# Optimization experiments

Hardware: AMD Instinct MI355X
Metric: run time of the kernel (lower is better)

The kernel has to match this reference:

```python
import jax, jax.numpy as jnp
import numpy as np

B, T, C_IN, H, W = 8, 12, 64, 64, 64
HID = 128
K = 3
NUM_CLASSES = 5


def _conv2d(x, w, b):
    # x: (B, Cin, H, W), w: (Cout, Cin, k, k) -> (B, Cout, H, W), SAME padding
    y = jax.lax.conv_general_dilated(
        x, w, window_strides=(1, 1), padding='SAME',
        dimension_numbers=('NCHW', 'OIHW', 'NCHW'))
    return y + b[None, :, None, None]


def setup_inputs() -> dict:
    key = jax.random.key(0)
    ks = jax.random.split(key, 5)
    inputs = jax.random.normal(ks[0], (B, T, C_IN, H, W), dtype=jnp.float32)
    # ConvLSTM gate conv: concat(x, h) channels -> 4*hidden gate channels
    fan_in = (C_IN + HID) * K * K
    w_lstm = jax.random.normal(ks[1], (4 * HID, C_IN + HID, K, K), dtype=jnp.float32) / np.sqrt(fan_in)
    b_lstm = jnp.zeros((4 * HID,), dtype=jnp.float32)
    w_conv = jax.random.normal(ks[2], (NUM_CLASSES, HID, K, K), dtype=jnp.float32) / np.sqrt(HID * K * K)
    b_conv = jnp.zeros((NUM_CLASSES,), dtype=jnp.float32)
    return {'inputs': inputs, 'w_lstm': w_lstm, 'b_lstm': b_lstm,
            'w_conv': w_conv, 'b_conv': b_conv}


def _clstm(inputs, w_lstm, b_lstm):
    # inputs: (B, T, C, H, W); returns final hidden state (B, HID, H, W)
    xs = jnp.transpose(inputs, (1, 0, 2, 3, 4))  # (T, B, C, H, W)
    h0 = jnp.zeros((inputs.shape[0], HID, H, W), dtype=inputs.dtype)
    c0 = jnp.zeros_like(h0)

    def step(carry, x_t):
        h, c = carry
        combined = jnp.concatenate([x_t, h], axis=1)           # (B, C+HID, H, W)
        gates = _conv2d(combined, w_lstm, b_lstm)              # (B, 4*HID, H, W)
        cc_i, cc_f, cc_o, cc_g = jnp.split(gates, 4, axis=1)
        i = jax.nn.sigmoid(cc_i)
        f = jax.nn.sigmoid(cc_f)
        o = jax.nn.sigmoid(cc_o)
        g = jnp.tanh(cc_g)
        c_next = f * c + i * g
        h_next = o * jnp.tanh(c_next)
        return (h_next, c_next), None

    (h_T, _), _ = jax.lax.scan(step, (h0, c0), xs)
    return h_T


def reference(inputs, w_lstm, b_lstm, w_conv, b_conv):
    final_state = _clstm(inputs, w_lstm, b_lstm)               # (B, HID, H, W)
    scores = _conv2d(final_state, w_conv, b_conv)              # (B, NUM_CLASSES, H, W)
    # Softmax2d over channels followed by log == channelwise log_softmax
    preds = jax.nn.log_softmax(scores, axis=1)
    return preds
```

## Files before the change

### kernel.cpp

```cpp
#include <hip/hip_runtime.h>
#include <math.h>

#define BB   8
#define TT   12

typedef _Float16 f16;
typedef f16  f16x8 __attribute__((ext_vector_type(8)));
typedef float f32x4 __attribute__((ext_vector_type(4)));

#define OFF_WT2  0ull
#define OFF_WC   1818624ull
#define OFF_XP   1855488ull
#define OFF_HA   6451200ull
#define OFF_HB   15642624ull
#define OFF_C    24834048ull
#define WS_END   41611264ull
#define ZERO_BYTES (WS_END - OFF_XP)

#define A_BYTES 43008
#define B_BYTES 37888

__device__ inline void gload16(const void* g, void* l) {
    __builtin_amdgcn_global_load_lds((const __attribute__((address_space(1))) void*)g,
                                     (__attribute__((address_space(3))) void*)l, 16, 0, 0);
}

__device__ inline float sigm_fast(float x) {
    return 1.f / (1.f + __expf(-x));
}
__device__ inline float tanh_fast(float x) {
    float xx = fminf(fmaxf(x, -15.f), 15.f);
    float e = __expf(2.f * xx);
    return (e - 1.f) / (e + 1.f);
}

__global__ __launch_bounds__(256) void zero_kernel(float4* __restrict__ p, int n4) {
    int i = blockIdx.x * blockDim.x + threadIdx.x;
    int stride = gridDim.x * blockDim.x;
    for (; i < n4; i += stride) p[i] = make_float4(0.f, 0.f, 0.f, 0.f);
}

__global__ __launch_bounds__(256) void wprep(const float* __restrict__ w, f16* __restrict__ wT2) {
    int t = blockIdx.x * 256 + threadIdx.x;
    if (t >= 8 * 6 * 64 * 296) return;
    int k    = t % 296;
    int r    = t / 296;
    int co_l = r & 63;
    int r2   = r >> 6;
    int chunk = r2 % 6;
    int ntl   = r2 / 6;
    f16 val = (f16)0.f;
    if (k < 288) {
        int tap = k >> 5, ci_l = k & 31;
        int ci  = chunk * 32 + ci_l;
        int cop = ntl * 64 + co_l;
        int hid = cop >> 2, gate = cop & 3;
        val = (f16)w[((size_t)(gate * 128 + hid) * 192 + ci) * 9 + tap];
    }
    wT2[t] = val;
}

__global__ __launch_bounds__(256) void wcprep(const float* __restrict__ w, float* __restrict__ wc) {
    int t = blockIdx.x * 256 + threadIdx.x;
    if (t >= 9216) return;
    int cls = t & 7, ci = (t >> 3) & 127, tap = t >> 10;
    wc[t] = (cls < 5) ? w[(size_t)(cls * 128 + ci) * 9 + tap] : 0.f;
}

__global__ __launch_bounds__(256) void xprep(const float* __restrict__ x, f16* __restrict__ xp, int t) {
    int pos = blockIdx.x * 256 + threadIdx.x;
    int b = pos >> 12, rr = pos & 4095, y = rr >> 6, xx = rr & 63;
    const float* s = x + ((size_t)(b * TT + t) * 64) * 4096 + y * 64 + xx;
    f16* d = xp + (((size_t)b * 66 + y + 1) * 68 + xx + 1) * 64;
    #pragma unroll
    for (int c8 = 0; c8 < 8; ++c8) {
        f16x8 v;
        #pragma unroll
        for (int e = 0; e < 8; ++e) v[e] = (f16)s[(size_t)(c8 * 8 + e) * 4096];
        *(f16x8*)&d[c8 * 8] = v;
    }
}

__device__ inline float pickc(f32x4 v, int j) {
    return j == 0 ? v[0] : j == 1 ? v[1] : j == 2 ? v[2] : v[3];
}

__global__ __launch_bounds__(256, 1) void gemm_step(
    const f16* __restrict__ xp, const f16* __restrict__ hin,
    const f16* __restrict__ wT2, const float* __restrict__ b_lstm,
    float* __restrict__ c_st, f16* __restrict__ hout)
{
    __shared__ __align__(16) char smem[2 * A_BYTES + 2 * B_BYTES];
    char* Ab0 = smem;
    char* Ab1 = smem + A_BYTES;
    char* Bb0 = smem + 2 * A_BYTES;
    char* Bb1 = smem + 2 * A_BYTES + B_BYTES;

    const int tid  = threadIdx.x;
    const int lane = tid & 63;
    const int wid  = tid >> 6;
    const int l15  = lane & 15, lg = lane >> 4;

    const int bid = blockIdx.x;
    const int nt  = bid >> 6;
    const int mt  = bid & 63;
    const int b   = mt >> 3;
    const int yr  = (mt & 7) << 3;

    const int rowbase = (b * 66 + yr) * 68;
    const f16* wslice = wT2 + (size_t)(nt * 6) * 18944;

    f32x4 acc[8][4] = {};

    int poA[11], cxA[11];
    #pragma unroll
    for (int i = 0; i < 11; ++i) {
        int k = wid + i * 4;
        int item = k * 64 + lane;
        int pc = item >> 2;
        int s  = item & 3;
        int pcc = pc < 660 ? pc : 0;
        int r = (pcc * 497) >> 15;
        int c = pcc - r * 66;
        poA[i] = rowbase + r * 68 + c;
        cxA[i] = (s ^ ((pcc >> 1) & 3)) * 8;
    }

    auto stageA = [&](int cc, char* Ad) {
        const f16* act; int sh, ci0;
        if (cc < 2) { act = xp;  sh = 6; ci0 = cc * 32; }
        else        { act = hin; sh = 7; ci0 = cc * 32 - 64; }
        #pragma unroll
        for (int i = 0; i < 11; ++i) {
            int k = wid + i * 4;
            if (k < 42)
                gload16(act + (((size_t)poA[i]) << sh) + ci0 + cxA[i], Ad + k * 1024);
        }
    };
    auto stageB = [&](int cc, char* Bd) {
        const char* bsrc = (const char*)(wslice + (size_t)cc * 18944);
        for (int k = wid; k < 37; k += 4)
            gload16(bsrc + k * 1024 + lane * 16, Bd + k * 1024);
    };
    auto compute = [&](const char* Abuf, const char* Bbuf) {
        const f16* As  = (const f16*)Abuf;
        const f16* Bsf = (const f16*)Bbuf;
        #pragma unroll
        for (int tap = 0; tap < 9; ++tap) {
            const int dy = tap / 3, dx = tap - dy * 3;
            f16x8 a[8];
            #pragma unroll
            for (int r2 = 0; r2 < 2; ++r2)
                #pragma unroll
                for (int mf = 0; mf < 4; ++mf) {
                    int p = (wid * 2 + r2 + dy) * 66 + mf * 16 + l15 + dx;
                    a[r2 * 4 + mf] = *(const f16x8*)&As[p * 32 + ((lg ^ ((p >> 1) & 3)) << 3)];
                }
            f16x8 bf[4];
            #pragma unroll
            for (int nf = 0; nf < 4; ++nf)
                bf[nf] = *(const f16x8*)&Bsf[(nf * 16 + l15) * 296 + tap * 32 + lg * 8];
            #pragma unroll
            for (int m = 0; m < 8; ++m)
                #pragma unroll
                for (int nf = 0; nf < 4; ++nf)
                    acc[m][nf] = __builtin_amdgcn_mfma_f32_16x16x32_f16(a[m], bf[nf], acc[m][nf], 0, 0, 0);
        }
    };

    stageA(0, Ab0);
    stageB(0, Bb0);
    __syncthreads();

    char* Ac = Ab0; char* Aa = Ab1;
    char* Bc = Bb0; char* Ba = Bb1;

    #pragma unroll 1
    for (int cc = 0; cc < 6; ++cc) {
        if (cc < 5) {
            stageA(cc + 1, Aa);
            stageB(cc + 1, Ba);
        }
        compute(Ac, Bc);
        __syncthreads();
        char* t1 = Ac; Ac = Aa; Aa = t1;
        char* t2 = Bc; Bc = Ba; Ba = t2;
    }

    const int q = lane & 3;
    #pragma unroll
    for (int m = 0; m < 8; ++m) {
        const int r2 = m >> 2, mf = m & 3;
        #pragma unroll
        for (int nf = 0; nf < 4; ++nf) {
            int hid = nt * 16 + nf * 4 + (l15 >> 2);
            float bias = b_lstm[q * 128 + hid];
            f32x4 v = acc[m][nf];
            v[0] += bias; v[1] += bias; v[2] += bias; v[3] += bias;
            float own = pickc(v, q);
            float r1 = __shfl_xor(pickc(v, q ^ 1), 1);
            float rr2 = __shfl_xor(pickc(v, q ^ 2), 2);
            float r3 = __shfl_xor(pickc(v, q ^ 3), 3);
            float gi = q == 0 ? own : (q == 1 ? r1 : q == 2 ? rr2 : r3);
            float gf = q == 1 ? own : (q == 0 ? r1 : q == 3 ? rr2 : r3);
            float go = q == 2 ? own : (q == 3 ? r1 : q == 0 ? rr2 : r3);
            float gg = q == 3 ? own : (q == 2 ? r1 : q == 1 ? rr2 : r3);
            float i_ = sigm_fast(gi);
            float f_ = sigm_fast(gf);
            float o_ = sigm_fast(go);
            float g_ = tanh_fast(gg);
            int px = mf * 16 + lg * 4 + q;
            int py = yr + wid * 2 + r2;
            size_t ic = (((size_t)b * 64 + py) * 64 + px) * 128 + hid;
            float cv = f_ * c_st[ic] + i_ * g_;
            c_st[ic] = cv;
            float hv = o_ * tanh_fast(cv);
            hout[(((size_t)b * 66 + py + 1) * 68 + (px + 1)) * 128 + hid] = (f16)hv;
        }
    }
}

__global__ __launch_bounds__(256) void final_conv(
    const f16* __restrict__ h, const float* __restrict__ wc,
    const float* __restrict__ b_conv, float* __restrict__ out)
{
    __shared__ float swc[9216];
    for (int i = threadIdx.x; i < 9216; i += 256) swc[i] = wc[i];
    __syncthreads();
    int pos = blockIdx.x * 256 + threadIdx.x;
    int b = pos >> 12, rr = pos & 4095, y = rr >> 6, xx = rr & 63;
    float acc[5];
    #pragma unroll
    for (int cls = 0; cls < 5; ++cls) acc[cls] = b_conv[cls];
    #pragma unroll 1
    for (int tap = 0; tap < 9; ++tap) {
        int dy = tap / 3, dx = tap - dy * 3;
        const f16* hp = h + (((size_t)b * 66 + y + dy) * 68 + xx + dx) * 128;
        #pragma unroll
        for (int c16 = 0; c16 < 16; ++c16) {
            f16x8 v = *(const f16x8*)&hp[c16 * 8];
            #pragma unroll
            for (int e = 0; e < 8; ++e) {
                float hv = (float)v[e];
                const float* wp = &swc[(size_t)(tap * 128 + c16 * 8 + e) * 8];
                acc[0] = fmaf(hv, wp[0], acc[0]);
                acc[1] = fmaf(hv, wp[1], acc[1]);
                acc[2] = fmaf(hv, wp[2], acc[2]);
                acc[3] = fmaf(hv, wp[3], acc[3]);
                acc[4] = fmaf(hv, wp[4], acc[4]);
            }
        }
    }
    float m = acc[0];
    #pragma unroll
    for (int cls = 1; cls < 5; ++cls) m = fmaxf(m, acc[cls]);
    float s = 0.f;
    #pragma unroll
    for (int cls = 0; cls < 5; ++cls) s += __expf(acc[cls] - m);
    float lse = logf(s) + m;
    #pragma unroll
    for (int cls = 0; cls < 5; ++cls)
        out[((size_t)(b * 5 + cls) << 12) + (y << 6) + xx] = acc[cls] - lse;
}

extern "C" void kernel_launch(void* const* d_in, const int* in_sizes, int n_in,
                              void* d_out, int out_size, void* d_ws, size_t ws_size,
                              hipStream_t stream) {
    const float* x      = (const float*)d_in[0];
    const float* w_lstm = (const float*)d_in[1];
    const float* b_lstm = (const float*)d_in[2];
    const float* w_conv = (const float*)d_in[3];
    const float* b_conv = (const float*)d_in[4];
    char* ws = (char*)d_ws;
    f16*   wT2 = (f16*)(ws + OFF_WT2);
    float* wc  = (float*)(ws + OFF_WC);
    f16*   xp  = (f16*)(ws + OFF_XP);
    f16*   hA  = (f16*)(ws + OFF_HA);
    f16*   hB  = (f16*)(ws + OFF_HB);
    float* c   = (float*)(ws + OFF_C);

    zero_kernel<<<2048, 256, 0, stream>>>((float4*)(ws + OFF_XP), (int)(ZERO_BYTES / 16));
    wprep<<<3552, 256, 0, stream>>>(w_lstm, wT2);
    wcprep<<<36, 256, 0, stream>>>(w_conv, wc);

    for (int t = 0; t < TT; ++t) {
        const f16* hin  = (t & 1) ? hB : hA;
        f16*       hout = (t & 1) ? hA : hB;
        xprep<<<128, 256, 0, stream>>>(x, xp, t);
        gemm_step<<<512, 256, 0, stream>>>(xp, hin, wT2, b_lstm, c, hout);
    }
    final_conv<<<128, 256, 0, stream>>>(hA, wc, b_conv, (float*)d_out);
}
```

Measured before the change: 1.037 ms.

## Double rows per block with 512 threads, single-buffer A tile

Each gemm_step block now covers 16 image rows instead of 8, using 8 waves and 256 blocks, so every weight slice loaded into shared memory serves twice as many output pixels and the halo rows are a smaller share of the input. To fit shared memory, the activation tile drops from double to single buffering: the next A chunk is loaded only after compute finishes, with an extra barrier, and only the weights stay double-buffered. This cuts weight traffic per pixel but exposes the A-load latency, and 256 blocks may leave some compute units idle.

```diff
diff --git a/kernel.cpp b/kernel.cpp
--- a/kernel.cpp
+++ b/kernel.cpp
@@ -17,7 +17,7 @@
 #define WS_END   41611264ull
 #define ZERO_BYTES (WS_END - OFF_XP)
 
-#define A_BYTES 43008
+#define A_BYTES 76800
 #define B_BYTES 37888
 
 __device__ inline void gload16(const void* g, void* l) {
@@ -85,16 +85,15 @@
     return j == 0 ? v[0] : j == 1 ? v[1] : j == 2 ? v[2] : v[3];
 }
 
-__global__ __launch_bounds__(256, 1) void gemm_step(
+__global__ __launch_bounds__(512, 1) void gemm_step(
     const f16* __restrict__ xp, const f16* __restrict__ hin,
     const f16* __restrict__ wT2, const float* __restrict__ b_lstm,
     float* __restrict__ c_st, f16* __restrict__ hout)
 {
-    __shared__ __align__(16) char smem[2 * A_BYTES + 2 * B_BYTES];
-    char* Ab0 = smem;
-    char* Ab1 = smem + A_BYTES;
-    char* Bb0 = smem + 2 * A_BYTES;
-    char* Bb1 = smem + 2 * A_BYTES + B_BYTES;
+    __shared__ __align__(16) char smem[A_BYTES + 2 * B_BYTES];
+    char* Ab  = smem;
+    char* Bb0 = smem + A_BYTES;
+    char* Bb1 = smem + A_BYTES + B_BYTES;
 
     const int tid  = threadIdx.x;
     const int lane = tid & 63;
@@ -102,48 +101,48 @@
     const int l15  = lane & 15, lg = lane >> 4;
 
     const int bid = blockIdx.x;
-    const int nt  = bid >> 6;
-    const int mt  = bid & 63;
-    const int b   = mt >> 3;
-    const int yr  = (mt & 7) << 3;
+    const int nt  = bid >> 5;
+    const int mt  = bid & 31;
+    const int b   = mt >> 2;
+    const int yr  = (mt & 3) << 4;
 
     const int rowbase = (b * 66 + yr) * 68;
     const f16* wslice = wT2 + (size_t)(nt * 6) * 18944;
 
     f32x4 acc[8][4] = {};
 
-    int poA[11], cxA[11];
-    #pragma unroll
-    for (int i = 0; i < 11; ++i) {
-        int k = wid + i * 4;
+    int poA[10], cxA[10];
+    #pragma unroll
+    for (int i = 0; i < 10; ++i) {
+        int k = wid + i * 8;
         int item = k * 64 + lane;
         int pc = item >> 2;
         int s  = item & 3;
-        int pcc = pc < 660 ? pc : 0;
-        int r = (pcc * 497) >> 15;
+        int pcc = pc < 1188 ? pc : 0;
+        int r = (pcc * 15888) >> 20;
         int c = pcc - r * 66;
         poA[i] = rowbase + r * 68 + c;
         cxA[i] = (s ^ ((pcc >> 1) & 3)) * 8;
     }
 
-    auto stageA = [&](int cc, char* Ad) {
+    auto stageA = [&](int cc) {
         const f16* act; int sh, ci0;
         if (cc < 2) { act = xp;  sh = 6; ci0 = cc * 32; }
         else        { act = hin; sh = 7; ci0 = cc * 32 - 64; }
         #pragma unroll
-        for (int i = 0; i < 11; ++i) {
-            int k = wid + i * 4;
-            if (k < 42)
-                gload16(act + (((size_t)poA[i]) << sh) + ci0 + cxA[i], Ad + k * 1024);
+        for (int i = 0; i < 10; ++i) {
+            int k = wid + i * 8;
+            if (k < 75)
+                gload16(act + (((size_t)poA[i]) << sh) + ci0 + cxA[i], Ab + k * 1024);
         }
     };
     auto stageB = [&](int cc, char* Bd) {
         const char* bsrc = (const char*)(wslice + (size_t)cc * 18944);
-        for (int k = wid; k < 37; k += 4)
+        for (int k = wid; k < 37; k += 8)
             gload16(bsrc + k * 1024 + lane * 16, Bd + k * 1024);
     };
-    auto compute = [&](const char* Abuf, const char* Bbuf) {
-        const f16* As  = (const f16*)Abuf;
+    auto compute = [&](const char* Bbuf) {
+        const f16* As  = (const f16*)Ab;
         const f16* Bsf = (const f16*)Bbuf;
         #pragma unroll
         for (int tap = 0; tap < 9; ++tap) {
@@ -168,22 +167,21 @@
         }
     };
 
-    stageA(0, Ab0);
+    stageA(0);
     stageB(0, Bb0);
     __syncthreads();
 
-    char* Ac = Ab0; char* Aa = Ab1;
     char* Bc = Bb0; char* Ba = Bb1;
 
     #pragma unroll 1
     for (int cc = 0; cc < 6; ++cc) {
+        if (cc < 5) stageB(cc + 1, Ba);
+        compute(Bc);
+        __syncthreads();
         if (cc < 5) {
-            stageA(cc + 1, Aa);
-            stageB(cc + 1, Ba);
-        }
-        compute(Ac, Bc);
-        __syncthreads();
-        char* t1 = Ac; Ac = Aa; Aa = t1;
+            stageA(cc + 1);
+            __syncthreads();
+        }
         char* t2 = Bc; Bc = Ba; Ba = t2;
     }
 
@@ -198,13 +196,13 @@
             f32x4 v = acc[m][nf];
             v[0] += bias; v[1] += bias; v[2] += bias; v[3] += bias;
             float own = pickc(v, q);
-            float r1 = __shfl_xor(pickc(v, q ^ 1), 1);
-            float rr2 = __shfl_xor(pickc(v, q ^ 2), 2);
-            float r3 = __shfl_xor(pickc(v, q ^ 3), 3);
-            float gi = q == 0 ? own : (q == 1 ? r1 : q == 2 ? rr2 : r3);
-            float gf = q == 1 ? own : (q == 0 ? r1 : q == 3 ? rr2 : r3);
-            float go = q == 2 ? own : (q == 3 ? r1 : q == 0 ? rr2 : r3);
-            float gg = q == 3 ? own : (q == 2 ? r1 : q == 1 ? rr2 : r3);
+            float s1 = __shfl_xor(pickc(v, q ^ 1), 1);
+            float s2 = __shfl_xor(pickc(v, q ^ 2), 2);
+            float s3 = __shfl_xor(pickc(v, q ^ 3), 3);
+            float gi = q == 0 ? own : (q == 1 ? s1 : q == 2 ? s2 : s3);
+            float gf = q == 1 ? own : (q == 0 ? s1 : q == 3 ? s2 : s3);
+            float go = q == 2 ? own : (q == 3 ? s1 : q == 0 ? s2 : s3);
+            float gg = q == 3 ? own : (q == 2 ? s1 : q == 1 ? s2 : s3);
             float i_ = sigm_fast(gi);
             float f_ = sigm_fast(gf);
             float o_ = sigm_fast(go);
@@ -287,7 +285,7 @@
         const f16* hin  = (t & 1) ? hB : hA;
         f16*       hout = (t & 1) ? hA : hB;
         xprep<<<128, 256, 0, stream>>>(x, xp, t);
-        gemm_step<<<512, 256, 0, stream>>>(xp, hin, wT2, b_lstm, c, hout);
+        gemm_step<<<256, 512, 0, stream>>>(xp, hin, wT2, b_lstm, c, hout);
     }
     final_conv<<<128, 256, 0, stream>>>(hA, wc, b_conv, (float*)d_out);
 }
```

New measurement: 872.8 us. 1.19x faster.
